# Performance work log

Hardware: AMD Instinct MI355X
Metric: run time of the kernel (lower is better)

The kernel has to match this reference:

```python
import jax, jax.numpy as jnp
import numpy as np

N = 50000      # number of 'stroke' nodes
E = 500000     # edges per edge type
IN = 256       # in_channels
OUT = 256      # out_channels


def setup_inputs() -> dict:
    key = jax.random.key(0)
    ks = jax.random.split(key, 6)
    x = jax.random.normal(ks[0], (N, IN), dtype=jnp.float32)
    edge_index_tp = jax.random.randint(ks[1], (2, E), 0, N, dtype=jnp.int64)
    edge_index_int = jax.random.randint(ks[2], (2, E), 0, N, dtype=jnp.int64)
    # Linear(2*IN, OUT) weights, torch default init scale ~ 1/sqrt(fan_in)
    scale = 1.0 / np.sqrt(2 * IN)
    W_tp = jax.random.uniform(ks[3], (OUT, 2 * IN), jnp.float32, -scale, scale)
    b_tp = jnp.zeros((OUT,), jnp.float32)
    W_int = jax.random.uniform(ks[4], (OUT, 2 * IN), jnp.float32, -scale, scale)
    b_int = jnp.zeros((OUT,), jnp.float32)
    return dict(x=x, edge_index_tp=edge_index_tp, edge_index_int=edge_index_int,
                W_tp=W_tp, b_tp=b_tp, W_int=W_int, b_int=b_int)


def _edge_conv(x, edge_index, W, b, aggr):
    # PyG EdgeConv: message = nn(concat[x_i, x_j - x_i]) for edge j->i,
    # nn = Linear(2*IN, OUT) + ReLU (MLPLinear with norm_type=None, act='relu')
    src, dst = edge_index[0], edge_index[1]
    x_i = x[dst]                     # [E, IN] target features
    x_j = x[src]                     # [E, IN] source features
    feat = jnp.concatenate([x_i, x_j - x_i], axis=-1)          # [E, 2*IN]
    msg = jax.nn.relu(feat @ W.T + b)                          # [E, OUT]
    n = x.shape[0]
    if aggr == 'sum':
        return jax.ops.segment_sum(msg, dst, num_segments=n)
    agg = jax.ops.segment_max(msg, dst, num_segments=n)
    # nodes with no incoming edges -> 0 (PyG scatter fill)
    return jnp.where(jnp.isfinite(agg), agg, 0.0)


def reference(x, edge_index_tp, edge_index_int, W_tp, b_tp, W_int, b_int):
    out_tp = _edge_conv(x, edge_index_tp, W_tp, b_tp, 'sum')    # temp_previous, aggr=sum
    out_int = _edge_conv(x, edge_index_int, W_int, b_int, 'max')  # intersects, aggr=max
    # HeteroConv(aggr='sum') over edge types targeting 'stroke'
    return out_tp + out_int
```

## Files before the change

kernel.cpp:

```cpp
#include <hip/hip_runtime.h>
#include <hip/hip_bf16.h>
#include <stdint.h>

#define NN 50000
#define EE 500000
#define NSCAT 487

typedef __attribute__((ext_vector_type(8))) short short8;
typedef __attribute__((ext_vector_type(4))) float f32x4;
typedef __attribute__((ext_vector_type(2))) float f32x2;
typedef __attribute__((ext_vector_type(4))) unsigned short u16x4;
typedef __attribute__((ext_vector_type(4))) unsigned int u32x4;

__device__ __forceinline__ unsigned short f2bf(float f) {
  union { float f; uint32_t u; } v; v.f = f;
  uint32_t u = v.u;
  return (unsigned short)((u + 0x7FFFu + ((u >> 16) & 1u)) >> 16);
}

__device__ __forceinline__ f32x4 bf4(const unsigned short* p) {
  u16x4 v = *(const u16x4*)p;
  f32x4 r;
  #pragma unroll
  for (int j = 0; j < 4; ++j) {
    union { uint32_t u; float f; } c; c.u = ((uint32_t)(unsigned short)v[j]) << 16; r[j] = c.f;
  }
  return r;
}

__device__ __forceinline__ f32x4 fp8x4(uint32_t v) {
  f32x2 lo = __builtin_amdgcn_cvt_pk_f32_fp8(v, false);
  f32x2 hi = __builtin_amdgcn_cvt_pk_f32_fp8(v, true);
  f32x4 r; r[0] = lo[0]; r[1] = lo[1]; r[2] = hi[0]; r[3] = hi[1];
  return r;
}

__global__ void k_prep0(const float* __restrict__ Wi, const float* __restrict__ Wt,
                        unsigned short* __restrict__ wtf, int* __restrict__ cnt) {
  const int b = blockIdx.x;
  if (b >= 1024) {
    const int idx = (b - 1024) * 2048 + threadIdx.x * 8;
    if (idx < 800000) {
      *(u32x4*)(cnt + idx) = (u32x4){0u, 0u, 0u, 0u};
      *(u32x4*)(cnt + idx + 4) = (u32x4){0u, 0u, 0u, 0u};
    }
    return;
  }
  const int i = b * 256 + threadIdx.x;
  const int o = i >> 8, k = i & 255;
  const float* W = (o < 512) ? Wi : Wt;
  const int oo = o & 511;
  const float v = (oo < 256) ? (W[oo * 512 + k] - W[oo * 512 + 256 + k])
                             : W[(oo - 256) * 512 + 256 + k];
  const int nt = o >> 8, wcv = (o >> 6) & 3, fn = (o >> 4) & 3, fl = o & 15;
  const int kt = k >> 5, fh = (k >> 3) & 3, j = k & 7;
  const int frag = (nt * 8 + kt) * 16 + wcv * 4 + fn;
  wtf[(size_t)frag * 512 + (fh * 16 + fl) * 8 + j] = f2bf(v);
}

#define SWZA(row, c) ((row) * 256 + ((((c) ^ ((row) & 7))) << 3))
#define SCR(row, c)  ((row) * 256 + ((((c) ^ ((row) & 7))) << 3))
#define SCR8(row, colb) ((row) * 256 + ((colb) ^ ((((row) >> 2) & 3) << 4)))

__device__ __forceinline__ void scat_edge(const int* __restrict__ e, int* __restrict__ cnt,
                                          unsigned short* __restrict__ so, int idx, int rep) {
  const int d = e[EE + idx];
  const int slot = atomicAdd(&cnt[rep * NN + d], 1);
  if (slot < 16) so[d * 128 + rep * 16 + slot] = (unsigned short)e[idx];
}

__launch_bounds__(256, 3)
__global__ void k_fused(const float* __restrict__ x, const unsigned short* __restrict__ wtf,
                        const float* __restrict__ b_int, const float* __restrict__ b_tp,
                        unsigned short* __restrict__ YA, unsigned char* __restrict__ Bi,
                        unsigned char* __restrict__ Bt, int M,
                        const int* __restrict__ ei, const int* __restrict__ et,
                        int* __restrict__ cnt_i, int* __restrict__ cnt_t,
                        unsigned short* __restrict__ so_i, unsigned short* __restrict__ so_t) {
  __shared__ unsigned short lA[64 * 256];
  __shared__ unsigned short scr[32 * 256];
  const int tid = threadIdx.x;
  const int g13 = blockIdx.x / 13, r13 = blockIdx.x % 13;

  if (r13 >= 8) {
    const int sid = g13 * 5 + (r13 - 8);
    const int rep = sid & 7;
    for (int idx = sid * 256 + tid; idx < EE; idx += NSCAT * 256)
      scat_edge(ei, cnt_i, so_i, idx, rep);
    for (int idx = sid * 256 + tid; idx < EE; idx += NSCAT * 256)
      scat_edge(et, cnt_t, so_t, idx, rep);
    return;
  }

  const int gid = g13 * 8 + r13;
  if (gid >= 782) return;
  const int lane = tid & 63;
  const int wc   = tid >> 6;
  const int row0 = gid * 64;
  const int fl = lane & 15, fh = lane >> 4;

  #pragma unroll
  for (int j = 0; j < 8; ++j) {
    const int cidx = j * 256 + tid;
    const int arow = cidx >> 5, c = cidx & 31;
    const int gr = min(row0 + arow, M - 1);
    const float* p = x + (size_t)gr * 256 + c * 8;
    const f32x4 lo = *(const f32x4*)p;
    const f32x4 hi = *(const f32x4*)(p + 4);
    short8 v;
    #pragma unroll
    for (int q = 0; q < 4; ++q) { v[q] = (short)f2bf(lo[q]); v[q + 4] = (short)f2bf(hi[q]); }
    *(short8*)(&lA[SWZA(arow, c)]) = v;
  }
  __syncthreads();

  for (int nt = 0; nt < 4; ++nt) {
    f32x4 acc[4][4];
    #pragma unroll
    for (int i = 0; i < 4; ++i)
      #pragma unroll
      for (int j = 0; j < 4; ++j) acc[i][j] = (f32x4){0.f, 0.f, 0.f, 0.f};

    #pragma unroll
    for (int kt = 0; kt < 8; ++kt) {
      const unsigned short* wbase = wtf + ((size_t)((nt * 8 + kt) * 16 + wc * 4)) * 512 + lane * 8;
      short8 af[4], bq[4];
      #pragma unroll
      for (int fn = 0; fn < 4; ++fn)
        bq[fn] = *(const short8*)(wbase + fn * 512);
      #pragma unroll
      for (int fm = 0; fm < 4; ++fm)
        af[fm] = *(const short8*)(&lA[SWZA(fm * 16 + fl, kt * 4 + fh)]);
      #pragma unroll
      for (int fm = 0; fm < 4; ++fm)
        #pragma unroll
        for (int fn = 0; fn < 4; ++fn)
          acc[fm][fn] = __builtin_amdgcn_mfma_f32_16x16x32_bf16(af[fm], bq[fn], acc[fm][fn], 0, 0, 0);
    }

    if ((nt & 1) == 0) {
      const float* bias = (nt == 0) ? b_int : b_tp;
      const int ycol0 = (nt == 0) ? 0 : 256;
      float bv[4];
      #pragma unroll
      for (int fn = 0; fn < 4; ++fn)
        bv[fn] = bias[wc * 64 + fn * 16 + fl];
      #pragma unroll
      for (int p = 0; p < 2; ++p) {
        __syncthreads();
        #pragma unroll
        for (int f2 = 0; f2 < 2; ++f2) {
          const int fm = p * 2 + f2;
          #pragma unroll
          for (int fn = 0; fn < 4; ++fn) {
            const int col = wc * 64 + fn * 16 + fl;
            #pragma unroll
            for (int r = 0; r < 4; ++r) {
              const int lr = f2 * 16 + fh * 4 + r;
              scr[SCR(lr, col >> 3) + (col & 7)] = f2bf(acc[fm][fn][r] + bv[fn]);
            }
          }
        }
        __syncthreads();
        const int tr = tid >> 3;
        const int grow = row0 + p * 32 + tr;
        if (grow < M) {
          #pragma unroll
          for (int j = 0; j < 4; ++j) {
            const int c = (tid & 7) + 8 * j;
            const short8 v = *(const short8*)(&scr[SCR(tr, c)]);
            *(short8*)(&YA[(size_t)grow * 512 + ycol0 + c * 8]) = v;
          }
        }
      }
    } else {
      unsigned char* dst = (nt == 1) ? Bi : Bt;
      unsigned char* s8 = (unsigned char*)scr;
      __syncthreads();
      #pragma unroll
      for (int fm = 0; fm < 4; ++fm) {
        const int rbase = fm * 16 + fh * 4;
        #pragma unroll
        for (int fn = 0; fn < 4; ++fn) {
          const int col = wc * 64 + fn * 16 + fl;
          const uint32_t p01 = __builtin_amdgcn_cvt_pk_fp8_f32(acc[fm][fn][0], acc[fm][fn][1], 0u, false);
          const uint32_t p23 = __builtin_amdgcn_cvt_pk_fp8_f32(acc[fm][fn][2], acc[fm][fn][3], 0u, false);
          s8[SCR8(rbase + 0, col)] = (unsigned char)(p01 & 0xFF);
          s8[SCR8(rbase + 1, col)] = (unsigned char)((p01 >> 8) & 0xFF);
          s8[SCR8(rbase + 2, col)] = (unsigned char)(p23 & 0xFF);
          s8[SCR8(rbase + 3, col)] = (unsigned char)((p23 >> 8) & 0xFF);
        }
      }
      __syncthreads();
      const int tr = tid >> 2;
      const int grow = row0 + tr;
      if (grow < M) {
        #pragma unroll
        for (int j = 0; j < 4; ++j) {
          const int c16 = ((tid & 3) + 4 * j) * 16;
          u32x4 w;
          #pragma unroll
          for (int d = 0; d < 4; ++d)
            w[d] = *(const uint32_t*)(s8 + SCR8(tr, c16) + d * 4);
          *(u32x4*)(dst + (size_t)grow * 256 + c16) = w;
        }
      }
      __syncthreads();
    }
  }
}

__global__ void k_agg2(const unsigned short* __restrict__ YA,
                       const uint32_t* __restrict__ Bi, const uint32_t* __restrict__ Bt,
                       const int* __restrict__ cnt_i, const int* __restrict__ cnt_t,
                       const uint32_t* __restrict__ so_i, const uint32_t* __restrict__ so_t,
                       float* __restrict__ out) {
  const int node = blockIdx.x * 4 + (threadIdx.x >> 6);
  if (node >= NN) return;
  const int lane = threadIdx.x & 63;
  const int c4 = lane << 2;

  const uint32_t bw_i = so_i[(size_t)node * 64 + lane];
  const uint32_t bw_t = so_t[(size_t)node * 64 + lane];
  int ncnt = 0;
  if (lane < 16) {
    const int* cp = (lane < 8) ? cnt_i : cnt_t;
    ncnt = cp[(lane & 7) * NN + node];
  }
  const f32x4 ai = bf4(YA + (size_t)node * 512 + c4);
  const f32x4 at = bf4(YA + (size_t)node * 512 + 256 + c4);

  f32x4 mx = (f32x4){0.f, 0.f, 0.f, 0.f};
  f32x4 sm = (f32x4){0.f, 0.f, 0.f, 0.f};

  #pragma unroll
  for (int r = 0; r < 8; ++r) {
    const int n = min(__shfl(ncnt, r), 16);
    int k = 0;
    for (; k + 2 <= n; k += 2) {
      const uint32_t w = (uint32_t)__shfl((int)bw_i, r * 8 + (k >> 1));
      const int s0 = w & 0xFFFF, s1 = w >> 16;
      const f32x4 b0 = fp8x4(Bi[(size_t)s0 * 64 + lane]);
      const f32x4 b1 = fp8x4(Bi[(size_t)s1 * 64 + lane]);
      #pragma unroll
      for (int j = 0; j < 4; ++j)
        mx[j] = fmaxf(mx[j], fmaxf(fmaxf(ai[j] + b0[j], 0.0f), fmaxf(ai[j] + b1[j], 0.0f)));
    }
    if (k < n) {
      const uint32_t w = (uint32_t)__shfl((int)bw_i, r * 8 + (k >> 1));
      const int s0 = w & 0xFFFF;
      const f32x4 b0 = fp8x4(Bi[(size_t)s0 * 64 + lane]);
      #pragma unroll
      for (int j = 0; j < 4; ++j) mx[j] = fmaxf(mx[j], fmaxf(ai[j] + b0[j], 0.0f));
    }
  }

  #pragma unroll
  for (int r = 0; r < 8; ++r) {
    const int n = min(__shfl(ncnt, r + 8), 16);
    int k = 0;
    for (; k + 2 <= n; k += 2) {
      const uint32_t w = (uint32_t)__shfl((int)bw_t, r * 8 + (k >> 1));
      const int s0 = w & 0xFFFF, s1 = w >> 16;
      const f32x4 b0 = fp8x4(Bt[(size_t)s0 * 64 + lane]);
      const f32x4 b1 = fp8x4(Bt[(size_t)s1 * 64 + lane]);
      #pragma unroll
      for (int j = 0; j < 4; ++j)
        sm[j] += fmaxf(at[j] + b0[j], 0.0f) + fmaxf(at[j] + b1[j], 0.0f);
    }
    if (k < n) {
      const uint32_t w = (uint32_t)__shfl((int)bw_t, r * 8 + (k >> 1));
      const int s0 = w & 0xFFFF;
      const f32x4 b0 = fp8x4(Bt[(size_t)s0 * 64 + lane]);
      #pragma unroll
      for (int j = 0; j < 4; ++j) sm[j] += fmaxf(at[j] + b0[j], 0.0f);
    }
  }

  f32x4 o;
  #pragma unroll
  for (int j = 0; j < 4; ++j) o[j] = mx[j] + sm[j];
  *(f32x4*)(out + (size_t)node * 256 + c4) = o;
}

extern "C" void kernel_launch(void* const* d_in, const int* in_sizes, int n_in,
                              void* d_out, int out_size, void* d_ws, size_t ws_size,
                              hipStream_t stream) {
  const float* x     = (const float*)d_in[0];
  const int*   e_tp  = (const int*)d_in[1];
  const int*   e_int = (const int*)d_in[2];
  const float* W_tp  = (const float*)d_in[3];
  const float* b_tp  = (const float*)d_in[4];
  const float* W_int = (const float*)d_in[5];
  const float* b_int = (const float*)d_in[6];
  float* out = (float*)d_out;

  char* w = (char*)d_ws;
  unsigned short* YA = (unsigned short*)w;
  unsigned char*  Bi = (unsigned char*)(w + 51200000);
  unsigned char*  Bt = (unsigned char*)(w + 64000000);
  int* cnt_i = (int*)(w + 76800000);
  int* cnt_t = (int*)(w + 78400000);
  unsigned short* so_i = (unsigned short*)(w + 80000000);
  unsigned short* so_t = (unsigned short*)(w + 92800000);
  unsigned short* wtf = (unsigned short*)(w + 105600000);

  k_prep0<<<1024 + 391, 256, 0, stream>>>(W_int, W_tp, wtf, cnt_i);
  k_fused<<<dim3(1271), dim3(256), 0, stream>>>(x, wtf, b_int, b_tp, YA, Bi, Bt, NN,
                                                e_int, e_tp, cnt_i, cnt_t, so_i, so_t);
  k_agg2<<<12500, 256, 0, stream>>>(YA, (const uint32_t*)Bi, (const uint32_t*)Bt,
                                    cnt_i, cnt_t, (const uint32_t*)so_i, (const uint32_t*)so_t, out);
}
```

Before: 151.5 us.

## Shrink epilogue scratch, double-buffer weight fragments, raise occupancy to four blocks

The epilogue scratch buffer is halved, so the bf16 output is staged 16 rows at a time and the fp8 output 32 rows at a time. This cuts LDS per block and allows launch bounds of 4 blocks per CU instead of 3. Weight fragments are now prefetched one k-step ahead into a double buffer, so global loads overlap the MFMAs, and the scatter replica index is taken from blockIdx instead of sid. The trade-off is more barriers per tile in the epilogue and register pressure from the extra B buffer under the tighter occupancy target, which risks spills.

```diff
diff --git a/kernel.cpp b/kernel.cpp
--- a/kernel.cpp
+++ b/kernel.cpp
@@ -59,7 +59,7 @@
 }
 
 #define SWZA(row, c) ((row) * 256 + ((((c) ^ ((row) & 7))) << 3))
-#define SCR(row, c)  ((row) * 256 + ((((c) ^ ((row) & 7))) << 3))
+#define SCR16(row, c) ((row) * 256 + ((((c) ^ ((row) & 7))) << 3))
 #define SCR8(row, colb) ((row) * 256 + ((colb) ^ ((((row) >> 2) & 3) << 4)))
 
 __device__ __forceinline__ void scat_edge(const int* __restrict__ e, int* __restrict__ cnt,
@@ -69,7 +69,7 @@
   if (slot < 16) so[d * 128 + rep * 16 + slot] = (unsigned short)e[idx];
 }
 
-__launch_bounds__(256, 3)
+__launch_bounds__(256, 4)
 __global__ void k_fused(const float* __restrict__ x, const unsigned short* __restrict__ wtf,
                         const float* __restrict__ b_int, const float* __restrict__ b_tp,
                         unsigned short* __restrict__ YA, unsigned char* __restrict__ Bi,
@@ -78,13 +78,13 @@
                         int* __restrict__ cnt_i, int* __restrict__ cnt_t,
                         unsigned short* __restrict__ so_i, unsigned short* __restrict__ so_t) {
   __shared__ unsigned short lA[64 * 256];
-  __shared__ unsigned short scr[32 * 256];
+  __shared__ unsigned short scr[16 * 256];
   const int tid = threadIdx.x;
   const int g13 = blockIdx.x / 13, r13 = blockIdx.x % 13;
 
   if (r13 >= 8) {
     const int sid = g13 * 5 + (r13 - 8);
-    const int rep = sid & 7;
+    const int rep = blockIdx.x & 7;
     for (int idx = sid * 256 + tid; idx < EE; idx += NSCAT * 256)
       scat_edge(ei, cnt_i, so_i, idx, rep);
     for (int idx = sid * 256 + tid; idx < EE; idx += NSCAT * 256)
@@ -98,6 +98,14 @@
   const int wc   = tid >> 6;
   const int row0 = gid * 64;
   const int fl = lane & 15, fh = lane >> 4;
+
+  short8 bq[2][4];
+  #define LOADB(s, buf) { \
+    const unsigned short* wb = wtf + ((size_t)((s) * 16 + wc * 4)) * 512 + lane * 8; \
+    _Pragma("unroll") \
+    for (int fn = 0; fn < 4; ++fn) buf[fn] = *(const short8*)(wb + fn * 512); }
+
+  LOADB(0, bq[0]);
 
   #pragma unroll
   for (int j = 0; j < 8; ++j) {
@@ -123,11 +131,13 @@
 
     #pragma unroll
     for (int kt = 0; kt < 8; ++kt) {
-      const unsigned short* wbase = wtf + ((size_t)((nt * 8 + kt) * 16 + wc * 4)) * 512 + lane * 8;
-      short8 af[4], bq[4];
-      #pragma unroll
-      for (int fn = 0; fn < 4; ++fn)
-        bq[fn] = *(const short8*)(wbase + fn * 512);
+      const int s = nt * 8 + kt;
+      if (kt < 7) {
+        LOADB(s + 1, bq[(kt & 1) ^ 1]);
+      } else if (nt < 3) {
+        LOADB(s + 1, bq[(kt & 1) ^ 1]);
+      }
+      short8 af[4];
       #pragma unroll
       for (int fm = 0; fm < 4; ++fm)
         af[fm] = *(const short8*)(&lA[SWZA(fm * 16 + fl, kt * 4 + fh)]);
@@ -135,7 +145,7 @@
       for (int fm = 0; fm < 4; ++fm)
         #pragma unroll
         for (int fn = 0; fn < 4; ++fn)
-          acc[fm][fn] = __builtin_amdgcn_mfma_f32_16x16x32_bf16(af[fm], bq[fn], acc[fm][fn], 0, 0, 0);
+          acc[fm][fn] = __builtin_amdgcn_mfma_f32_16x16x32_bf16(af[fm], bq[kt & 1][fn], acc[fm][fn], 0, 0, 0);
     }
 
     if ((nt & 1) == 0) {
@@ -145,20 +155,49 @@
       #pragma unroll
       for (int fn = 0; fn < 4; ++fn)
         bv[fn] = bias[wc * 64 + fn * 16 + fl];
+      #pragma unroll
+      for (int p = 0; p < 4; ++p) {
+        __syncthreads();
+        #pragma unroll
+        for (int fn = 0; fn < 4; ++fn) {
+          const int col = wc * 64 + fn * 16 + fl;
+          #pragma unroll
+          for (int r = 0; r < 4; ++r) {
+            const int lr = fh * 4 + r;
+            scr[SCR16(lr, col >> 3) + (col & 7)] = f2bf(acc[p][fn][r] + bv[fn]);
+          }
+        }
+        __syncthreads();
+        const int tr = tid >> 4;
+        const int grow = row0 + p * 16 + tr;
+        if (grow < M) {
+          #pragma unroll
+          for (int j = 0; j < 2; ++j) {
+            const int c = (tid & 15) + 16 * j;
+            const short8 v = *(const short8*)(&scr[SCR16(tr, c)]);
+            *(short8*)(&YA[(size_t)grow * 512 + ycol0 + c * 8]) = v;
+          }
+        }
+      }
+    } else {
+      unsigned char* dst = (nt == 1) ? Bi : Bt;
+      unsigned char* s8 = (unsigned char*)scr;
       #pragma unroll
       for (int p = 0; p < 2; ++p) {
         __syncthreads();
         #pragma unroll
         for (int f2 = 0; f2 < 2; ++f2) {
           const int fm = p * 2 + f2;
+          const int rbase = f2 * 16 + fh * 4;
           #pragma unroll
           for (int fn = 0; fn < 4; ++fn) {
             const int col = wc * 64 + fn * 16 + fl;
-            #pragma unroll
-            for (int r = 0; r < 4; ++r) {
-              const int lr = f2 * 16 + fh * 4 + r;
-              scr[SCR(lr, col >> 3) + (col & 7)] = f2bf(acc[fm][fn][r] + bv[fn]);
-            }
+            const uint32_t p01 = __builtin_amdgcn_cvt_pk_fp8_f32(acc[fm][fn][0], acc[fm][fn][1], 0u, false);
+            const uint32_t p23 = __builtin_amdgcn_cvt_pk_fp8_f32(acc[fm][fn][2], acc[fm][fn][3], 0u, false);
+            s8[SCR8(rbase + 0, col)] = (unsigned char)(p01 & 0xFF);
+            s8[SCR8(rbase + 1, col)] = (unsigned char)((p01 >> 8) & 0xFF);
+            s8[SCR8(rbase + 2, col)] = (unsigned char)(p23 & 0xFF);
+            s8[SCR8(rbase + 3, col)] = (unsigned char)((p23 >> 8) & 0xFF);
           }
         }
         __syncthreads();
@@ -166,48 +205,20 @@
         const int grow = row0 + p * 32 + tr;
         if (grow < M) {
           #pragma unroll
-          for (int j = 0; j < 4; ++j) {
-            const int c = (tid & 7) + 8 * j;
-            const short8 v = *(const short8*)(&scr[SCR(tr, c)]);
-            *(short8*)(&YA[(size_t)grow * 512 + ycol0 + c * 8]) = v;
+          for (int j = 0; j < 2; ++j) {
+            const int c16 = ((tid & 7) * 2 + j) * 16;
+            u32x4 w;
+            #pragma unroll
+            for (int d = 0; d < 4; ++d)
+              w[d] = *(const uint32_t*)(s8 + SCR8(tr, c16) + d * 4);
+            *(u32x4*)(dst + (size_t)grow * 256 + c16) = w;
           }
         }
       }
-    } else {
-      unsigned char* dst = (nt == 1) ? Bi : Bt;
-      unsigned char* s8 = (unsigned char*)scr;
-      __syncthreads();
-      #pragma unroll
-      for (int fm = 0; fm < 4; ++fm) {
-        const int rbase = fm * 16 + fh * 4;
-        #pragma unroll
-        for (int fn = 0; fn < 4; ++fn) {
-          const int col = wc * 64 + fn * 16 + fl;
-          const uint32_t p01 = __builtin_amdgcn_cvt_pk_fp8_f32(acc[fm][fn][0], acc[fm][fn][1], 0u, false);
-          const uint32_t p23 = __builtin_amdgcn_cvt_pk_fp8_f32(acc[fm][fn][2], acc[fm][fn][3], 0u, false);
-          s8[SCR8(rbase + 0, col)] = (unsigned char)(p01 & 0xFF);
-          s8[SCR8(rbase + 1, col)] = (unsigned char)((p01 >> 8) & 0xFF);
-          s8[SCR8(rbase + 2, col)] = (unsigned char)(p23 & 0xFF);
-          s8[SCR8(rbase + 3, col)] = (unsigned char)((p23 >> 8) & 0xFF);
-        }
-      }
-      __syncthreads();
-      const int tr = tid >> 2;
-      const int grow = row0 + tr;
-      if (grow < M) {
-        #pragma unroll
-        for (int j = 0; j < 4; ++j) {
-          const int c16 = ((tid & 3) + 4 * j) * 16;
-          u32x4 w;
-          #pragma unroll
-          for (int d = 0; d < 4; ++d)
-            w[d] = *(const uint32_t*)(s8 + SCR8(tr, c16) + d * 4);
-          *(u32x4*)(dst + (size_t)grow * 256 + c16) = w;
-        }
-      }
-      __syncthreads();
-    }
-  }
+      if (nt == 1) __syncthreads();
+    }
+  }
+  #undef LOADB
 }
 
 __global__ void k_agg2(const unsigned short* __restrict__ YA,
```

After: 192.7 us. +27.2%, slower.

## Interleave edge scatter chunks into GEMM blocks instead of dedicated scatter blocks

Applied to the files above, without the earlier changes.

Removes the separate scatter-only blocks in the fused kernel. Each of the 782 GEMM blocks now handles 1280 edges, processed in five chunks placed between its x-load and N-tile phases, so the atomic scatter latency can overlap MFMA work. This cuts the grid size and spreads the scatter evenly across blocks. In exchange, the GEMM blocks carry extra memory traffic and atomics on their critical path, and replica selection now follows the block id.

```diff
diff --git a/kernel.cpp b/kernel.cpp
--- a/kernel.cpp
+++ b/kernel.cpp
@@ -4,7 +4,7 @@
 
 #define NN 50000
 #define EE 500000
-#define NSCAT 487
+#define NGB 782
 
 typedef __attribute__((ext_vector_type(8))) short short8;
 typedef __attribute__((ext_vector_type(4))) float f32x4;
@@ -61,13 +61,6 @@
 #define SWZA(row, c) ((row) * 256 + ((((c) ^ ((row) & 7))) << 3))
 #define SCR(row, c)  ((row) * 256 + ((((c) ^ ((row) & 7))) << 3))
 #define SCR8(row, colb) ((row) * 256 + ((colb) ^ ((((row) >> 2) & 3) << 4)))
-
-__device__ __forceinline__ void scat_edge(const int* __restrict__ e, int* __restrict__ cnt,
-                                          unsigned short* __restrict__ so, int idx, int rep) {
-  const int d = e[EE + idx];
-  const int slot = atomicAdd(&cnt[rep * NN + d], 1);
-  if (slot < 16) so[d * 128 + rep * 16 + slot] = (unsigned short)e[idx];
-}
 
 __launch_bounds__(256, 3)
 __global__ void k_fused(const float* __restrict__ x, const unsigned short* __restrict__ wtf,
@@ -80,24 +73,26 @@
   __shared__ unsigned short lA[64 * 256];
   __shared__ unsigned short scr[32 * 256];
   const int tid = threadIdx.x;
-  const int g13 = blockIdx.x / 13, r13 = blockIdx.x % 13;
-
-  if (r13 >= 8) {
-    const int sid = g13 * 5 + (r13 - 8);
-    const int rep = sid & 7;
-    for (int idx = sid * 256 + tid; idx < EE; idx += NSCAT * 256)
-      scat_edge(ei, cnt_i, so_i, idx, rep);
-    for (int idx = sid * 256 + tid; idx < EE; idx += NSCAT * 256)
-      scat_edge(et, cnt_t, so_t, idx, rep);
-    return;
-  }
-
-  const int gid = g13 * 8 + r13;
-  if (gid >= 782) return;
+  const int gid = blockIdx.x;
   const int lane = tid & 63;
   const int wc   = tid >> 6;
   const int row0 = gid * 64;
   const int fl = lane & 15, fh = lane >> 4;
+  const int rep = gid & 7;
+
+  auto chunk = [&](int p) {
+    const int v = gid * 1280 + p * 256 + tid;
+    if (v < EE) {
+      const int d = ei[EE + v];
+      const int slot = atomicAdd(&cnt_i[rep * NN + d], 1);
+      if (slot < 16) so_i[d * 128 + rep * 16 + slot] = (unsigned short)ei[v];
+    } else if (v < 2 * EE) {
+      const int vv = v - EE;
+      const int d = et[EE + vv];
+      const int slot = atomicAdd(&cnt_t[rep * NN + d], 1);
+      if (slot < 16) so_t[d * 128 + rep * 16 + slot] = (unsigned short)et[vv];
+    }
+  };
 
   #pragma unroll
   for (int j = 0; j < 8; ++j) {
@@ -112,6 +107,7 @@
     for (int q = 0; q < 4; ++q) { v[q] = (short)f2bf(lo[q]); v[q + 4] = (short)f2bf(hi[q]); }
     *(short8*)(&lA[SWZA(arow, c)]) = v;
   }
+  chunk(0);
   __syncthreads();
 
   for (int nt = 0; nt < 4; ++nt) {
@@ -207,6 +203,7 @@
       }
       __syncthreads();
     }
+    chunk(nt + 1);
   }
 }
 
@@ -306,8 +303,8 @@
   unsigned short* wtf = (unsigned short*)(w + 105600000);
 
   k_prep0<<<1024 + 391, 256, 0, stream>>>(W_int, W_tp, wtf, cnt_i);
-  k_fused<<<dim3(1271), dim3(256), 0, stream>>>(x, wtf, b_int, b_tp, YA, Bi, Bt, NN,
-                                                e_int, e_tp, cnt_i, cnt_t, so_i, so_t);
+  k_fused<<<dim3(NGB), dim3(256), 0, stream>>>(x, wtf, b_int, b_tp, YA, Bi, Bt, NN,
+                                               e_int, e_tp, cnt_i, cnt_t, so_i, so_t);
   k_agg2<<<12500, 256, 0, stream>>>(YA, (const uint32_t*)Bi, (const uint32_t*)Bt,
                                     cnt_i, cnt_t, (const uint32_t*)so_i, (const uint32_t*)so_t, out);
 }
```

Result: slower. 155.8 us (+2.8%).
